# Kernel tuning notes

Hardware: AMD Instinct MI355X
Metric: run time of the kernel (lower is better)

## Reference

```python
import jax, jax.numpy as jnp
import numpy as np


def setup_inputs() -> dict:
    key = jax.random.key(0)
    k1, k2, k3 = jax.random.split(key, 3)
    L, B, D = 2048, 32, 512  # seq_len, batch, input_size == hidden_size == output_size
    NUM_MATRICES = 3  # has_skip_term and input_size == output_size
    x = jax.random.normal(k1, (L, B, D), dtype=jnp.float32)
    # transform_module: Linear(D, D * 3, bias=False), xavier_uniform-like scale
    W = jax.random.normal(k2, (D, D * NUM_MATRICES), dtype=jnp.float32) * (1.0 / np.sqrt(D))
    # weight_c ~ U(-weight_c_init, weight_c_init), shape (2*D,)
    weight_c = jax.random.uniform(k3, (2 * D,), dtype=jnp.float32, minval=-1.0, maxval=1.0)
    # bias: zeros; highway_bias (=0.0) added to second half -> all zeros
    bias = jnp.zeros((2 * D,), dtype=jnp.float32)
    return {"x": x, "W": W, "weight_c": weight_c, "bias": bias}


def reference(x, W, weight_c, bias):
    # x: (L, B, D); W: (D, 3D); weight_c, bias: (2D,)
    L, B, D = x.shape
    # U = transform_module(x): batched matmul, then view as (L, B, D, 3)
    U = jnp.einsum('lbi,io->lbo', x, W).reshape(L, B, D, 3)
    wc_f, wc_r = weight_c[:D], weight_c[D:]  # forget / reset peephole weights
    b_f, b_r = bias[:D], bias[D:]            # forget / reset (highway) biases

    def step(c_prev, inp):
        u, res = inp  # u: (B, D, 3); res: (B, D) residual (= x_t, skip term)
        fg = jax.nn.sigmoid(u[..., 1] + wc_f * c_prev + b_f)
        rg = jax.nn.sigmoid(u[..., 2] + wc_r * c_prev + b_r)
        c = fg * c_prev + (1.0 - fg) * u[..., 0]
        # activation_type == 0 -> g(c) = c; scale_val is None (rescale=False)
        h = rg * c + (1.0 - rg) * res
        return c, h

    c0 = jnp.zeros((B, D), dtype=x.dtype)
    c_last, h = jax.lax.scan(step, c0, (U, x))
    return h, c_last
```

## Files before the change

### kernel.cpp

```cpp
#include <hip/hip_runtime.h>

#define LL 2048
#define BB 32
#define DD 512
#define NN (3 * DD)
#define KK (DD)

#define SCH 16
#define NCH (LL / SCH)

typedef short bf16x8 __attribute__((ext_vector_type(8)));
typedef float f32x4 __attribute__((ext_vector_type(4)));

__device__ __forceinline__ unsigned short f2bf(float f) {
  unsigned u = __builtin_bit_cast(unsigned, f);
  u += 0x7fffu + ((u >> 16) & 1u);
  return (unsigned short)(u >> 16);
}

__global__ __launch_bounds__(256) void cvt_w_kernel(const float* __restrict__ W,
                                                    unsigned short* __restrict__ Wt) {
  int j = blockIdx.x * 256 + threadIdx.x;
  int i  = j & (KK - 1);
  int op = j >> 9;
  int g  = op >> 9;
  int dd = op & (DD - 1);
  Wt[j] = f2bf(W[(size_t)i * NN + dd * 3 + g]);
}

__global__ __launch_bounds__(448, 4) void fused_kernel(
    const float* __restrict__ x, const unsigned short* __restrict__ Wt,
    const float* __restrict__ wc, const float* __restrict__ bias,
    float* __restrict__ out) {
  __shared__ __align__(16) unsigned short xbuf[2][SCH * DD];
  __shared__ __align__(16) float ubuf[2][SCH][112];
  __shared__ __align__(16) float rbuf[4][SCH][32];

  const int n   = blockIdx.x;
  const int xcd = n & 7;
  const int idx = n >> 3;
  const int b   = xcd * 4 + (idx >> 4);
  const int d0  = (idx & 15) << 5;

  const int wv   = threadIdx.x >> 6;
  const int lane = threadIdx.x & 63;

  if (wv < 6) {
    const int quad = lane >> 4;
    const int l16  = lane & 15;
    bf16x8 wfrag[16];
    {
      const int row = (wv >> 1) * DD + d0 + (wv & 1) * 16 + l16;
      const unsigned short* wp = Wt + (size_t)row * KK + quad * 8;
#pragma unroll
      for (int j = 0; j < 16; ++j)
        wfrag[j] = *(const bf16x8*)(wp + j * 32);
    }
    const int gl    = wv * 64 + lane;
    const int abase = l16 * 1024;
    const int aswz  = (l16 & 7) << 4;
    const int c16lo = d0 >> 3;

    for (int s = 0; s <= NCH + 1; ++s) {
      float4 st0a, st0b, st1a, st1b, st2a, st2b;
      const bool do_stage = (s < NCH);
      const bool t2 = (gl < 256);
      if (do_stage) {
        {
          int row = gl >> 6, c16 = gl & 63;
          const float* sp = x + ((size_t)(s * SCH + row) * BB + b) * DD + c16 * 8;
          st0a = *(const float4*)sp; st0b = *(const float4*)(sp + 4);
        }
        {
          int bid = 384 + gl; int row = bid >> 6, c16 = bid & 63;
          const float* sp = x + ((size_t)(s * SCH + row) * BB + b) * DD + c16 * 8;
          st1a = *(const float4*)sp; st1b = *(const float4*)(sp + 4);
        }
        if (t2) {
          int bid = 768 + gl; int row = bid >> 6, c16 = bid & 63;
          const float* sp = x + ((size_t)(s * SCH + row) * BB + b) * DD + c16 * 8;
          st2a = *(const float4*)sp; st2b = *(const float4*)(sp + 4);
        }
      }
      if (s >= 1 && s <= NCH) {
        const char* xb = (const char*)xbuf[(s - 1) & 1];
        f32x4 acc = {};
#pragma unroll
        for (int j = 0; j < 16; ++j) {
          bf16x8 af = *(const bf16x8*)(xb + abase + ((j * 64 + quad * 16) ^ aswz));
          acc = __builtin_amdgcn_mfma_f32_16x16x32_bf16(af, wfrag[j], acc, 0, 0, 0);
        }
        float* up = &ubuf[(s - 1) & 1][0][0];
#pragma unroll
        for (int r = 0; r < 4; ++r)
          up[(quad * 4 + r) * 112 + wv * 16 + l16] = acc[r];
      }
      if (do_stage) {
        char*  xw = (char*)xbuf[s & 1];
        float* rw = &rbuf[s & 3][0][0];
        {
          int row = gl >> 6, c16 = gl & 63;
          int cg = c16 - c16lo;
          if ((unsigned)cg < 4u) {
            *(float4*)&rw[row * 32 + cg * 8]     = st0a;
            *(float4*)&rw[row * 32 + cg * 8 + 4] = st0b;
          }
          union { bf16x8 v; unsigned short u[8]; } o;
          o.u[0]=f2bf(st0a.x); o.u[1]=f2bf(st0a.y); o.u[2]=f2bf(st0a.z); o.u[3]=f2bf(st0a.w);
          o.u[4]=f2bf(st0b.x); o.u[5]=f2bf(st0b.y); o.u[6]=f2bf(st0b.z); o.u[7]=f2bf(st0b.w);
          *(bf16x8*)(xw + row * 1024 + ((c16 * 16) ^ ((row & 7) << 4))) = o.v;
        }
        {
          int bid = 384 + gl; int row = bid >> 6, c16 = bid & 63;
          int cg = c16 - c16lo;
          if ((unsigned)cg < 4u) {
            *(float4*)&rw[row * 32 + cg * 8]     = st1a;
            *(float4*)&rw[row * 32 + cg * 8 + 4] = st1b;
          }
          union { bf16x8 v; unsigned short u[8]; } o;
          o.u[0]=f2bf(st1a.x); o.u[1]=f2bf(st1a.y); o.u[2]=f2bf(st1a.z); o.u[3]=f2bf(st1a.w);
          o.u[4]=f2bf(st1b.x); o.u[5]=f2bf(st1b.y); o.u[6]=f2bf(st1b.z); o.u[7]=f2bf(st1b.w);
          *(bf16x8*)(xw + row * 1024 + ((c16 * 16) ^ ((row & 7) << 4))) = o.v;
        }
        if (t2) {
          int bid = 768 + gl; int row = bid >> 6, c16 = bid & 63;
          int cg = c16 - c16lo;
          if ((unsigned)cg < 4u) {
            *(float4*)&rw[row * 32 + cg * 8]     = st2a;
            *(float4*)&rw[row * 32 + cg * 8 + 4] = st2b;
          }
          union { bf16x8 v; unsigned short u[8]; } o;
          o.u[0]=f2bf(st2a.x); o.u[1]=f2bf(st2a.y); o.u[2]=f2bf(st2a.z); o.u[3]=f2bf(st2a.w);
          o.u[4]=f2bf(st2b.x); o.u[5]=f2bf(st2b.y); o.u[6]=f2bf(st2b.z); o.u[7]=f2bf(st2b.w);
          *(bf16x8*)(xw + row * 1024 + ((c16 * 16) ^ ((row & 7) << 4))) = o.v;
        }
      }
      __syncthreads();
    }
  } else {
    const int ch = lane;
    const float kln = 1.442695040888963f;
    float pf0 = 0.f, pr0 = 0.f, pf1 = 0.f, pr1 = 0.f, c = 0.f;
    float* hp = nullptr;
    if (ch < 32) {
      const int d = d0 + ch;
      float wcf = wc[d], wcr = wc[DD + d];
      pf0 = -kln * bias[d];      pr0 = -kln * bias[DD + d];
      pf1 = -kln * wcf;          pr1 = -kln * wcr;
      hp = out + (size_t)b * DD + d;
    }
    for (int s = 0; s <= NCH + 1; ++s) {
      if (s >= 2 && ch < 32) {
        const int cc = s - 2;
        const float* ub = &ubuf[cc & 1][0][0];
        const float* rb = &rbuf[cc & 3][0][0];
        float u0v[SCH], u1v[SCH], u2v[SCH], xrv[SCH];
#pragma unroll
        for (int t = 0; t < SCH; ++t) {
          u0v[t] = ub[t * 112 + ch];
          u1v[t] = ub[t * 112 + 32 + ch];
          u2v[t] = ub[t * 112 + 64 + ch];
          xrv[t] = rb[t * 32 + ch];
        }
#pragma unroll
        for (int t = 0; t < SCH; ++t) {
          float tf = __builtin_fmaf(pf1, c, __builtin_fmaf(-kln, u1v[t], pf0));
          float tr = __builtin_fmaf(pr1, c, __builtin_fmaf(-kln, u2v[t], pr0));
          float fg = __builtin_amdgcn_rcpf(1.0f + __builtin_amdgcn_exp2f(tf));
          float rg = __builtin_amdgcn_rcpf(1.0f + __builtin_amdgcn_exp2f(tr));
          c = __builtin_fmaf(fg, c - u0v[t], u0v[t]);
          *hp = __builtin_fmaf(rg, c - xrv[t], xrv[t]);
          hp += BB * DD;
        }
      }
      __syncthreads();
    }
    if (ch < 32)
      out[(size_t)LL * BB * DD + (size_t)b * DD + d0 + ch] = c;
  }
}

extern "C" void kernel_launch(void* const* d_in, const int* in_sizes, int n_in,
                              void* d_out, int out_size, void* d_ws, size_t ws_size,
                              hipStream_t stream) {
  const float* x    = (const float*)d_in[0];
  const float* W    = (const float*)d_in[1];
  const float* wc   = (const float*)d_in[2];
  const float* bias = (const float*)d_in[3];
  float* out = (float*)d_out;

  unsigned short* Wt = (unsigned short*)d_ws;

  cvt_w_kernel<<<(NN * KK) / 256, 256, 0, stream>>>(W, Wt);
  fused_kernel<<<BB * (DD / 32), 448, 0, stream>>>(x, Wt, wc, bias, out);
}
```

Before: 453.8 us.

## Shrink block to 3 MFMA waves with two accumulators and transposed U buffer

Cuts the block from 7 waves to 4: 3 MFMA waves each compute two 16-column tiles with two accumulators instead of 6 waves computing one tile each, and staging loads are spread across fewer threads. The U shared buffer is transposed to channel-major with padding, so MFMA results are stored as vector writes and the scan wave reads float4s. The aim is higher occupancy with fewer waves per block and cheaper LDS traffic, at the cost of more registers per MFMA wave and more staging work per thread.

```diff
diff --git a/kernel.cpp b/kernel.cpp
--- a/kernel.cpp
+++ b/kernel.cpp
@@ -8,6 +8,7 @@
 
 #define SCH 16
 #define NCH (LL / SCH)
+#define TP 20
 
 typedef short bf16x8 __attribute__((ext_vector_type(8)));
 typedef float f32x4 __attribute__((ext_vector_type(4)));
@@ -28,12 +29,12 @@
   Wt[j] = f2bf(W[(size_t)i * NN + dd * 3 + g]);
 }
 
-__global__ __launch_bounds__(448, 4) void fused_kernel(
+__global__ __launch_bounds__(256, 2) void fused_kernel(
     const float* __restrict__ x, const unsigned short* __restrict__ Wt,
     const float* __restrict__ wc, const float* __restrict__ bias,
     float* __restrict__ out) {
   __shared__ __align__(16) unsigned short xbuf[2][SCH * DD];
-  __shared__ __align__(16) float ubuf[2][SCH][112];
+  __shared__ __align__(16) float ubt[2][3][32][TP];
   __shared__ __align__(16) float rbuf[4][SCH][32];
 
   const int n   = blockIdx.x;
@@ -45,16 +46,18 @@
   const int wv   = threadIdx.x >> 6;
   const int lane = threadIdx.x & 63;
 
-  if (wv < 6) {
+  if (wv < 3) {
     const int quad = lane >> 4;
     const int l16  = lane & 15;
-    bf16x8 wfrag[16];
+    bf16x8 wf0[16], wf1[16];
     {
-      const int row = (wv >> 1) * DD + d0 + (wv & 1) * 16 + l16;
-      const unsigned short* wp = Wt + (size_t)row * KK + quad * 8;
+      const unsigned short* wp0 = Wt + (size_t)(wv * DD + d0 + l16) * KK + quad * 8;
+      const unsigned short* wp1 = wp0 + (size_t)16 * KK;
 #pragma unroll
-      for (int j = 0; j < 16; ++j)
-        wfrag[j] = *(const bf16x8*)(wp + j * 32);
+      for (int j = 0; j < 16; ++j) {
+        wf0[j] = *(const bf16x8*)(wp0 + j * 32);
+        wf1[j] = *(const bf16x8*)(wp1 + j * 32);
+      }
     }
     const int gl    = wv * 64 + lane;
     const int abase = l16 * 1024;
@@ -62,76 +65,65 @@
     const int c16lo = d0 >> 3;
 
     for (int s = 0; s <= NCH + 1; ++s) {
-      float4 st0a, st0b, st1a, st1b, st2a, st2b;
+      float4 sa[6], sb[6];
       const bool do_stage = (s < NCH);
-      const bool t2 = (gl < 256);
+      const bool t6 = (gl < 64);
       if (do_stage) {
-        {
-          int row = gl >> 6, c16 = gl & 63;
+#pragma unroll
+        for (int i = 0; i < 5; ++i) {
+          int bid = gl + 192 * i;
+          int row = bid >> 6, c16 = bid & 63;
           const float* sp = x + ((size_t)(s * SCH + row) * BB + b) * DD + c16 * 8;
-          st0a = *(const float4*)sp; st0b = *(const float4*)(sp + 4);
+          sa[i] = *(const float4*)sp; sb[i] = *(const float4*)(sp + 4);
         }
-        {
-          int bid = 384 + gl; int row = bid >> 6, c16 = bid & 63;
+        if (t6) {
+          int bid = 960 + gl;
+          int row = bid >> 6, c16 = bid & 63;
           const float* sp = x + ((size_t)(s * SCH + row) * BB + b) * DD + c16 * 8;
-          st1a = *(const float4*)sp; st1b = *(const float4*)(sp + 4);
-        }
-        if (t2) {
-          int bid = 768 + gl; int row = bid >> 6, c16 = bid & 63;
-          const float* sp = x + ((size_t)(s * SCH + row) * BB + b) * DD + c16 * 8;
-          st2a = *(const float4*)sp; st2b = *(const float4*)(sp + 4);
+          sa[5] = *(const float4*)sp; sb[5] = *(const float4*)(sp + 4);
         }
       }
       if (s >= 1 && s <= NCH) {
         const char* xb = (const char*)xbuf[(s - 1) & 1];
-        f32x4 acc = {};
+        f32x4 acc0 = {}, acc1 = {};
 #pragma unroll
         for (int j = 0; j < 16; ++j) {
           bf16x8 af = *(const bf16x8*)(xb + abase + ((j * 64 + quad * 16) ^ aswz));
-          acc = __builtin_amdgcn_mfma_f32_16x16x32_bf16(af, wfrag[j], acc, 0, 0, 0);
+          acc0 = __builtin_amdgcn_mfma_f32_16x16x32_bf16(af, wf0[j], acc0, 0, 0, 0);
+          acc1 = __builtin_amdgcn_mfma_f32_16x16x32_bf16(af, wf1[j], acc1, 0, 0, 0);
         }
-        float* up = &ubuf[(s - 1) & 1][0][0];
-#pragma unroll
-        for (int r = 0; r < 4; ++r)
-          up[(quad * 4 + r) * 112 + wv * 16 + l16] = acc[r];
+        float* ug = &ubt[(s - 1) & 1][wv][0][0];
+        *(f32x4*)&ug[l16 * TP + quad * 4]        = acc0;
+        *(f32x4*)&ug[(16 + l16) * TP + quad * 4] = acc1;
       }
       if (do_stage) {
         char*  xw = (char*)xbuf[s & 1];
         float* rw = &rbuf[s & 3][0][0];
-        {
-          int row = gl >> 6, c16 = gl & 63;
+#pragma unroll
+        for (int i = 0; i < 5; ++i) {
+          int bid = gl + 192 * i;
+          int row = bid >> 6, c16 = bid & 63;
           int cg = c16 - c16lo;
           if ((unsigned)cg < 4u) {
-            *(float4*)&rw[row * 32 + cg * 8]     = st0a;
-            *(float4*)&rw[row * 32 + cg * 8 + 4] = st0b;
+            *(float4*)&rw[row * 32 + cg * 8]     = sa[i];
+            *(float4*)&rw[row * 32 + cg * 8 + 4] = sb[i];
           }
           union { bf16x8 v; unsigned short u[8]; } o;
-          o.u[0]=f2bf(st0a.x); o.u[1]=f2bf(st0a.y); o.u[2]=f2bf(st0a.z); o.u[3]=f2bf(st0a.w);
-          o.u[4]=f2bf(st0b.x); o.u[5]=f2bf(st0b.y); o.u[6]=f2bf(st0b.z); o.u[7]=f2bf(st0b.w);
+          o.u[0]=f2bf(sa[i].x); o.u[1]=f2bf(sa[i].y); o.u[2]=f2bf(sa[i].z); o.u[3]=f2bf(sa[i].w);
+          o.u[4]=f2bf(sb[i].x); o.u[5]=f2bf(sb[i].y); o.u[6]=f2bf(sb[i].z); o.u[7]=f2bf(sb[i].w);
           *(bf16x8*)(xw + row * 1024 + ((c16 * 16) ^ ((row & 7) << 4))) = o.v;
         }
-        {
-          int bid = 384 + gl; int row = bid >> 6, c16 = bid & 63;
+        if (t6) {
+          int bid = 960 + gl;
+          int row = bid >> 6, c16 = bid & 63;
           int cg = c16 - c16lo;
           if ((unsigned)cg < 4u) {
-            *(float4*)&rw[row * 32 + cg * 8]     = st1a;
-            *(float4*)&rw[row * 32 + cg * 8 + 4] = st1b;
+            *(float4*)&rw[row * 32 + cg * 8]     = sa[5];
+            *(float4*)&rw[row * 32 + cg * 8 + 4] = sb[5];
           }
           union { bf16x8 v; unsigned short u[8]; } o;
-          o.u[0]=f2bf(st1a.x); o.u[1]=f2bf(st1a.y); o.u[2]=f2bf(st1a.z); o.u[3]=f2bf(st1a.w);
-          o.u[4]=f2bf(st1b.x); o.u[5]=f2bf(st1b.y); o.u[6]=f2bf(st1b.z); o.u[7]=f2bf(st1b.w);
-          *(bf16x8*)(xw + row * 1024 + ((c16 * 16) ^ ((row & 7) << 4))) = o.v;
-        }
-        if (t2) {
-          int bid = 768 + gl; int row = bid >> 6, c16 = bid & 63;
-          int cg = c16 - c16lo;
-          if ((unsigned)cg < 4u) {
-            *(float4*)&rw[row * 32 + cg * 8]     = st2a;
-            *(float4*)&rw[row * 32 + cg * 8 + 4] = st2b;
-          }
-          union { bf16x8 v; unsigned short u[8]; } o;
-          o.u[0]=f2bf(st2a.x); o.u[1]=f2bf(st2a.y); o.u[2]=f2bf(st2a.z); o.u[3]=f2bf(st2a.w);
-          o.u[4]=f2bf(st2b.x); o.u[5]=f2bf(st2b.y); o.u[6]=f2bf(st2b.z); o.u[7]=f2bf(st2b.w);
+          o.u[0]=f2bf(sa[5].x); o.u[1]=f2bf(sa[5].y); o.u[2]=f2bf(sa[5].z); o.u[3]=f2bf(sa[5].w);
+          o.u[4]=f2bf(sb[5].x); o.u[5]=f2bf(sb[5].y); o.u[6]=f2bf(sb[5].z); o.u[7]=f2bf(sb[5].w);
           *(bf16x8*)(xw + row * 1024 + ((c16 * 16) ^ ((row & 7) << 4))) = o.v;
         }
       }
@@ -152,16 +144,20 @@
     for (int s = 0; s <= NCH + 1; ++s) {
       if (s >= 2 && ch < 32) {
         const int cc = s - 2;
-        const float* ub = &ubuf[cc & 1][0][0];
+        const float* ub = &ubt[cc & 1][0][0][0];
         const float* rb = &rbuf[cc & 3][0][0];
         float u0v[SCH], u1v[SCH], u2v[SCH], xrv[SCH];
 #pragma unroll
-        for (int t = 0; t < SCH; ++t) {
-          u0v[t] = ub[t * 112 + ch];
-          u1v[t] = ub[t * 112 + 32 + ch];
-          u2v[t] = ub[t * 112 + 64 + ch];
-          xrv[t] = rb[t * 32 + ch];
+        for (int j = 0; j < 4; ++j) {
+          float4 q0 = *(const float4*)&ub[        ch * TP + j * 4];
+          float4 q1 = *(const float4*)&ub[ 640 +  ch * TP + j * 4];
+          float4 q2 = *(const float4*)&ub[1280 +  ch * TP + j * 4];
+          u0v[j*4+0]=q0.x; u0v[j*4+1]=q0.y; u0v[j*4+2]=q0.z; u0v[j*4+3]=q0.w;
+          u1v[j*4+0]=q1.x; u1v[j*4+1]=q1.y; u1v[j*4+2]=q1.z; u1v[j*4+3]=q1.w;
+          u2v[j*4+0]=q2.x; u2v[j*4+1]=q2.y; u2v[j*4+2]=q2.z; u2v[j*4+3]=q2.w;
         }
+#pragma unroll
+        for (int t = 0; t < SCH; ++t) xrv[t] = rb[t * 32 + ch];
 #pragma unroll
         for (int t = 0; t < SCH; ++t) {
           float tf = __builtin_fmaf(pf1, c, __builtin_fmaf(-kln, u1v[t], pf0));
@@ -192,5 +188,5 @@
   unsigned short* Wt = (unsigned short*)d_ws;
 
   cvt_w_kernel<<<(NN * KK) / 256, 256, 0, stream>>>(W, Wt);
-  fused_kernel<<<BB * (DD / 32), 448, 0, stream>>>(x, Wt, wc, bias, out);
+  fused_kernel<<<BB * (DD / 32), 256, 0, stream>>>(x, Wt, wc, bias, out);
 }
```

New measurement: 412.1 us. 9.2% less time.
